# Performance work log

Measured on AMD Instinct MI355X. Metric: run time of the kernel, lower is better.

Reference implementation:

```python
import jax, jax.numpy as jnp
import numpy as np

ROUTING_ITERS = 3
EPS = 1e-07


def setup_inputs() -> dict:
    key = jax.random.key(0)
    k1, k2 = jax.random.split(key)
    B, IN_CAPS, OUT_CAPS, POSE = 128, 2048, 32, 4
    votes = jax.random.normal(k1, (B, IN_CAPS, OUT_CAPS, POSE), dtype=jnp.float32)
    activations_in = jax.random.uniform(k2, (B, IN_CAPS), dtype=jnp.float32)
    return {"votes": votes, "activations_in": activations_in}


def _safe_norm(s, axis=-1):
    # NOTE: original safe_norm always keeps dims (reduce_sum keepdims=True, then sqrt)
    return jnp.sqrt(jnp.sum(jnp.square(s), axis=axis, keepdims=True) + EPS)


def _squash(s):
    s_norm = _safe_norm(s, axis=-1)                 # [..., 1]
    scale = jnp.square(s_norm) / (1.0 + jnp.square(s_norm))
    return scale * (s / s_norm)


def reference(votes, activations_in):
    # votes: [B, in_caps, out_caps, pose]
    B, in_caps, out_caps, _ = votes.shape
    b_ij = jnp.zeros((B, in_caps, out_caps), dtype=jnp.float32)
    v_j = None
    for _ in range(ROUTING_ITERS):
        c_ij = jax.nn.softmax(b_ij, axis=2)                       # [B, I, O]
        s_j = jnp.einsum('bio,biop->bop', c_ij, votes)            # [B, O, P]
        v_j = _squash(s_j)                                        # [B, O, P]
        v_stop = jax.lax.stop_gradient(v_j)
        agreement = jnp.einsum('biop,bop->bio', votes, v_stop)    # [B, I, O]
        b_ij = b_ij + agreement
    poses_out = v_j                                               # [B, O, P]
    activations_out = _safe_norm(poses_out, axis=-1)              # [B, O, 1] (keepdims bug preserved)
    return poses_out, activations_out
```

## Files before the change

kernel.cpp:

```cpp
#include <hip/hip_runtime.h>


#define BATCH 128
#define IC 2048
#define OC 32
#define POSE 4
#define REPS 1e-7f
#define CHUNKS 16
#define CHUNK_I (IC / CHUNKS)
#define BLOCK_T 256
#define GROUPS (BLOCK_T / 32)
#define ILP 4
#define STEPS (CHUNK_I / (GROUPS * ILP))

__device__ __forceinline__ float dot4(const float4 a, const float4 b) {
    return a.x*b.x + a.y*b.y + a.z*b.z + a.w*b.w;
}

__device__ __forceinline__ float4 squash4(const float4 s) {
    const float n2 = s.x*s.x + s.y*s.y + s.z*s.z + s.w*s.w + REPS;
    const float f = n2 / (1.f + n2) * rsqrtf(n2);
    return make_float4(f*s.x, f*s.y, f*s.z, f*s.w);
}

template <int T>
__global__ __launch_bounds__(BLOCK_T) void routing_accum(
    const float4* __restrict__ votes,
    const float4* __restrict__ s_all,
    float* __restrict__ s_out)
{
    const int blk   = blockIdx.x;
    const int b     = blk >> 4;
    const int chunk = blk & (CHUNKS - 1);
    const int o     = threadIdx.x & 31;
    const int g     = threadIdx.x >> 5;

    float4 vh0 = make_float4(0.f, 0.f, 0.f, 0.f);
    float4 vh1 = make_float4(0.f, 0.f, 0.f, 0.f);
    if (T >= 1) vh0 = squash4(s_all[0 * BATCH * OC + b * OC + o]);
    if (T >= 2) vh1 = squash4(s_all[1 * BATCH * OC + b * OC + o]);

    float4 s_acc = make_float4(0.f, 0.f, 0.f, 0.f);

    const float4* vb = votes + (size_t)b * IC * OC;
    const int i0 = chunk * CHUNK_I;

    #pragma unroll
    for (int step = 0; step < STEPS; ++step) {
        const int ia = i0 + step * (GROUPS * ILP) + g;
        float4 v0 = vb[(size_t)(ia + 0 * GROUPS) * OC + o];
        float4 v1 = vb[(size_t)(ia + 1 * GROUPS) * OC + o];
        float4 v2 = vb[(size_t)(ia + 2 * GROUPS) * OC + o];
        float4 v3 = vb[(size_t)(ia + 3 * GROUPS) * OC + o];

        if (T == 0) {
            s_acc.x += (v0.x + v1.x) + (v2.x + v3.x);
            s_acc.y += (v0.y + v1.y) + (v2.y + v3.y);
            s_acc.z += (v0.z + v1.z) + (v2.z + v3.z);
            s_acc.w += (v0.w + v1.w) + (v2.w + v3.w);
        } else {
            float l0 = dot4(v0, vh0);
            float l1 = dot4(v1, vh0);
            float l2 = dot4(v2, vh0);
            float l3 = dot4(v3, vh0);
            if (T >= 2) {
                l0 += dot4(v0, vh1); l1 += dot4(v1, vh1);
                l2 += dot4(v2, vh1); l3 += dot4(v3, vh1);
            }
            float e0 = __expf(l0), e1 = __expf(l1), e2 = __expf(l2), e3 = __expf(l3);
            float t0 = e0, t1 = e1, t2 = e2, t3 = e3;
            #pragma unroll
            for (int d = 16; d >= 1; d >>= 1) {
                t0 += __shfl_xor(t0, d);
                t1 += __shfl_xor(t1, d);
                t2 += __shfl_xor(t2, d);
                t3 += __shfl_xor(t3, d);
            }
            const float c0 = e0 * __builtin_amdgcn_rcpf(t0);
            const float c1 = e1 * __builtin_amdgcn_rcpf(t1);
            const float c2 = e2 * __builtin_amdgcn_rcpf(t2);
            const float c3 = e3 * __builtin_amdgcn_rcpf(t3);

            s_acc.x += c0*v0.x + c1*v1.x + c2*v2.x + c3*v3.x;
            s_acc.y += c0*v0.y + c1*v1.y + c2*v2.y + c3*v3.y;
            s_acc.z += c0*v0.z + c1*v1.z + c2*v2.z + c3*v3.z;
            s_acc.w += c0*v0.w + c1*v1.w + c2*v2.w + c3*v3.w;
        }
    }

    __shared__ float4 lds_s[GROUPS * 32];
    lds_s[g * 32 + o] = s_acc;
    __syncthreads();

    if (threadIdx.x < 32) {
        float4 tot = lds_s[o];
        #pragma unroll
        for (int gg = 1; gg < GROUPS; ++gg) {
            const float4 x = lds_s[gg * 32 + o];
            tot.x += x.x; tot.y += x.y; tot.z += x.z; tot.w += x.w;
        }
        if (T == 0) {
            const float inv = 1.f / 32.f;
            tot.x *= inv; tot.y *= inv; tot.z *= inv; tot.w *= inv;
        }
        float* dst = s_out + ((size_t)b * OC + o) * 4;
        atomicAdd(dst + 0, tot.x);
        atomicAdd(dst + 1, tot.y);
        atomicAdd(dst + 2, tot.z);
        atomicAdd(dst + 3, tot.w);
    }
}

__global__ void routing_finalize(
    const float4* __restrict__ s2,
    float* __restrict__ out)
{
    const int idx = blockIdx.x * blockDim.x + threadIdx.x;
    if (idx >= BATCH * OC) return;
    const float4 v = squash4(s2[idx]);
    ((float4*)out)[idx] = v;
    const float a = sqrtf(v.x*v.x + v.y*v.y + v.z*v.z + v.w*v.w + REPS);
    out[BATCH * OC * POSE + idx] = a;
}

extern "C" void kernel_launch(void* const* d_in, const int* in_sizes, int n_in,
                              void* d_out, int out_size, void* d_ws, size_t ws_size,
                              hipStream_t stream) {
    const float4* votes = (const float4*)d_in[0];

    float* s_all = (float*)d_ws;

    hipMemsetAsync(s_all, 0, (size_t)3 * BATCH * OC * 4 * sizeof(float), stream);

    const float4* s_all4 = (const float4*)s_all;
    routing_accum<0><<<BATCH * CHUNKS, BLOCK_T, 0, stream>>>(
        votes, s_all4, s_all + 0 * BATCH * OC * 4);
    routing_accum<1><<<BATCH * CHUNKS, BLOCK_T, 0, stream>>>(
        votes, s_all4, s_all + 1 * BATCH * OC * 4);
    routing_accum<2><<<BATCH * CHUNKS, BLOCK_T, 0, stream>>>(
        votes, s_all4, s_all + 2 * BATCH * OC * 4);
    routing_finalize<<<(BATCH * OC + 255) / 256, 256, 0, stream>>>(
        s_all4 + 2 * BATCH * OC, (float*)d_out);
}
```

Measured before the change: 236.7 us.

## Fuse routing passes into one cooperative kernel with grid-wide syncs

Replaces the memset, three accumulation launches and the finalize launch with a single cooperative kernel of 1024 blocks. The blocks zero the workspace, then run the three routing passes with grid.sync barriers between them and finalize the outputs in place. This removes the per-launch overhead and the separate memset, and drops ILP from 4 to 2 to fit the new block count. The cost is several grid-wide barriers, and the kernel only works if all 1024 blocks can be resident at once.

```diff
diff --git a/kernel.cpp b/kernel.cpp
--- a/kernel.cpp
+++ b/kernel.cpp
@@ -1,4 +1,7 @@
 #include <hip/hip_runtime.h>
+#include <hip/hip_cooperative_groups.h>
+
+namespace cg = cooperative_groups;
 
 
 #define BATCH 128
@@ -6,11 +9,12 @@
 #define OC 32
 #define POSE 4
 #define REPS 1e-7f
-#define CHUNKS 16
+#define NBLK 1024
+#define CHUNKS (NBLK / BATCH)
 #define CHUNK_I (IC / CHUNKS)
 #define BLOCK_T 256
 #define GROUPS (BLOCK_T / 32)
-#define ILP 4
+#define ILP 2
 #define STEPS (CHUNK_I / (GROUPS * ILP))
 
 __device__ __forceinline__ float dot4(const float4 a, const float4 b) {
@@ -23,75 +27,49 @@
     return make_float4(f*s.x, f*s.y, f*s.z, f*s.w);
 }
 
+__device__ __forceinline__ float4 load4(const float* p) {
+    return *(const float4*)p;
+}
+
 template <int T>
-__global__ __launch_bounds__(BLOCK_T) void routing_accum(
-    const float4* __restrict__ votes,
-    const float4* __restrict__ s_all,
-    float* __restrict__ s_out)
+__device__ __forceinline__ float4 accum_pass(
+    const float4* __restrict__ vb, int i0, int g, int o,
+    float4 vh0, float4 vh1)
 {
-    const int blk   = blockIdx.x;
-    const int b     = blk >> 4;
-    const int chunk = blk & (CHUNKS - 1);
-    const int o     = threadIdx.x & 31;
-    const int g     = threadIdx.x >> 5;
-
-    float4 vh0 = make_float4(0.f, 0.f, 0.f, 0.f);
-    float4 vh1 = make_float4(0.f, 0.f, 0.f, 0.f);
-    if (T >= 1) vh0 = squash4(s_all[0 * BATCH * OC + b * OC + o]);
-    if (T >= 2) vh1 = squash4(s_all[1 * BATCH * OC + b * OC + o]);
-
-    float4 s_acc = make_float4(0.f, 0.f, 0.f, 0.f);
-
-    const float4* vb = votes + (size_t)b * IC * OC;
-    const int i0 = chunk * CHUNK_I;
-
-    #pragma unroll
+    float4 s = make_float4(0.f, 0.f, 0.f, 0.f);
+    #pragma unroll 4
     for (int step = 0; step < STEPS; ++step) {
         const int ia = i0 + step * (GROUPS * ILP) + g;
-        float4 v0 = vb[(size_t)(ia + 0 * GROUPS) * OC + o];
-        float4 v1 = vb[(size_t)(ia + 1 * GROUPS) * OC + o];
-        float4 v2 = vb[(size_t)(ia + 2 * GROUPS) * OC + o];
-        float4 v3 = vb[(size_t)(ia + 3 * GROUPS) * OC + o];
-
+        const float4 v0 = vb[(size_t)ia * OC + o];
+        const float4 v1 = vb[(size_t)(ia + GROUPS) * OC + o];
         if (T == 0) {
-            s_acc.x += (v0.x + v1.x) + (v2.x + v3.x);
-            s_acc.y += (v0.y + v1.y) + (v2.y + v3.y);
-            s_acc.z += (v0.z + v1.z) + (v2.z + v3.z);
-            s_acc.w += (v0.w + v1.w) + (v2.w + v3.w);
+            s.x += v0.x + v1.x; s.y += v0.y + v1.y;
+            s.z += v0.z + v1.z; s.w += v0.w + v1.w;
         } else {
             float l0 = dot4(v0, vh0);
             float l1 = dot4(v1, vh0);
-            float l2 = dot4(v2, vh0);
-            float l3 = dot4(v3, vh0);
-            if (T >= 2) {
-                l0 += dot4(v0, vh1); l1 += dot4(v1, vh1);
-                l2 += dot4(v2, vh1); l3 += dot4(v3, vh1);
-            }
-            float e0 = __expf(l0), e1 = __expf(l1), e2 = __expf(l2), e3 = __expf(l3);
-            float t0 = e0, t1 = e1, t2 = e2, t3 = e3;
+            if (T >= 2) { l0 += dot4(v0, vh1); l1 += dot4(v1, vh1); }
+            float e0 = __expf(l0), e1 = __expf(l1);
+            float t0 = e0, t1 = e1;
             #pragma unroll
             for (int d = 16; d >= 1; d >>= 1) {
                 t0 += __shfl_xor(t0, d);
                 t1 += __shfl_xor(t1, d);
-                t2 += __shfl_xor(t2, d);
-                t3 += __shfl_xor(t3, d);
             }
             const float c0 = e0 * __builtin_amdgcn_rcpf(t0);
             const float c1 = e1 * __builtin_amdgcn_rcpf(t1);
-            const float c2 = e2 * __builtin_amdgcn_rcpf(t2);
-            const float c3 = e3 * __builtin_amdgcn_rcpf(t3);
-
-            s_acc.x += c0*v0.x + c1*v1.x + c2*v2.x + c3*v3.x;
-            s_acc.y += c0*v0.y + c1*v1.y + c2*v2.y + c3*v3.y;
-            s_acc.z += c0*v0.z + c1*v1.z + c2*v2.z + c3*v3.z;
-            s_acc.w += c0*v0.w + c1*v1.w + c2*v2.w + c3*v3.w;
+            s.x += c0*v0.x + c1*v1.x; s.y += c0*v0.y + c1*v1.y;
+            s.z += c0*v0.z + c1*v1.z; s.w += c0*v0.w + c1*v1.w;
         }
     }
+    return s;
+}
 
-    __shared__ float4 lds_s[GROUPS * 32];
-    lds_s[g * 32 + o] = s_acc;
+__device__ __forceinline__ void reduce_atomic(
+    float4 p, float4* lds_s, float* dst_base, int g, int o, float scale)
+{
+    lds_s[g * 32 + o] = p;
     __syncthreads();
-
     if (threadIdx.x < 32) {
         float4 tot = lds_s[o];
         #pragma unroll
@@ -99,46 +77,82 @@
             const float4 x = lds_s[gg * 32 + o];
             tot.x += x.x; tot.y += x.y; tot.z += x.z; tot.w += x.w;
         }
-        if (T == 0) {
-            const float inv = 1.f / 32.f;
-            tot.x *= inv; tot.y *= inv; tot.z *= inv; tot.w *= inv;
-        }
-        float* dst = s_out + ((size_t)b * OC + o) * 4;
-        atomicAdd(dst + 0, tot.x);
-        atomicAdd(dst + 1, tot.y);
-        atomicAdd(dst + 2, tot.z);
-        atomicAdd(dst + 3, tot.w);
+        float* dst = dst_base + o * 4;
+        atomicAdd(dst + 0, tot.x * scale);
+        atomicAdd(dst + 1, tot.y * scale);
+        atomicAdd(dst + 2, tot.z * scale);
+        atomicAdd(dst + 3, tot.w * scale);
     }
 }
 
-__global__ void routing_finalize(
-    const float4* __restrict__ s2,
+__global__ __launch_bounds__(BLOCK_T, 8) void routing_fused(
+    const float4* __restrict__ votes,
+    float* __restrict__ s_all,
     float* __restrict__ out)
 {
-    const int idx = blockIdx.x * blockDim.x + threadIdx.x;
-    if (idx >= BATCH * OC) return;
-    const float4 v = squash4(s2[idx]);
-    ((float4*)out)[idx] = v;
-    const float a = sqrtf(v.x*v.x + v.y*v.y + v.z*v.z + v.w*v.w + REPS);
-    out[BATCH * OC * POSE + idx] = a;
+    cg::grid_group grid = cg::this_grid();
+
+    const int blk   = blockIdx.x;
+    const int b     = blk >> 3;
+    const int chunk = blk & (CHUNKS - 1);
+    const int o     = threadIdx.x & 31;
+    const int g     = threadIdx.x >> 5;
+
+    if (threadIdx.x < 48) s_all[blk * 48 + threadIdx.x] = 0.f;
+
+    __shared__ float4 lds_s[GROUPS * 32];
+
+    const float4* vb = votes + (size_t)b * IC * OC;
+    const int i0 = chunk * CHUNK_I;
+
+    float4 vh0 = make_float4(0.f, 0.f, 0.f, 0.f);
+    float4 vh1 = vh0;
+
+    float4 p = accum_pass<0>(vb, i0, g, o, vh0, vh1);
+    lds_s[g * 32 + o] = p;
+    grid.sync();
+    if (threadIdx.x < 32) {
+        float4 tot = lds_s[o];
+        #pragma unroll
+        for (int gg = 1; gg < GROUPS; ++gg) {
+            const float4 x = lds_s[gg * 32 + o];
+            tot.x += x.x; tot.y += x.y; tot.z += x.z; tot.w += x.w;
+        }
+        float* dst = s_all + 0 * BATCH * OC * 4 + (b * OC + o) * 4;
+        const float inv = 1.f / 32.f;
+        atomicAdd(dst + 0, tot.x * inv);
+        atomicAdd(dst + 1, tot.y * inv);
+        atomicAdd(dst + 2, tot.z * inv);
+        atomicAdd(dst + 3, tot.w * inv);
+    }
+    grid.sync();
+
+    vh0 = squash4(load4(s_all + 0 * BATCH * OC * 4 + (b * OC + o) * 4));
+    p = accum_pass<1>(vb, i0, g, o, vh0, vh1);
+    reduce_atomic(p, lds_s, s_all + 1 * BATCH * OC * 4 + b * OC * 4, g, o, 1.f);
+    grid.sync();
+
+    vh1 = squash4(load4(s_all + 1 * BATCH * OC * 4 + (b * OC + o) * 4));
+    p = accum_pass<2>(vb, i0, g, o, vh0, vh1);
+    reduce_atomic(p, lds_s, s_all + 2 * BATCH * OC * 4 + b * OC * 4, g, o, 1.f);
+    grid.sync();
+
+    if (chunk == 0 && threadIdx.x < 32) {
+        const float4 v = squash4(load4(s_all + 2 * BATCH * OC * 4 + (b * OC + o) * 4));
+        ((float4*)out)[b * OC + o] = v;
+        const float a = sqrtf(v.x*v.x + v.y*v.y + v.z*v.z + v.w*v.w + REPS);
+        out[BATCH * OC * POSE + b * OC + o] = a;
+    }
 }
 
 extern "C" void kernel_launch(void* const* d_in, const int* in_sizes, int n_in,
                               void* d_out, int out_size, void* d_ws, size_t ws_size,
                               hipStream_t stream) {
     const float4* votes = (const float4*)d_in[0];
+    float* s_all = (float*)d_ws;
+    float* outp  = (float*)d_out;
 
-    float* s_all = (float*)d_ws;
-
-    hipMemsetAsync(s_all, 0, (size_t)3 * BATCH * OC * 4 * sizeof(float), stream);
-
-    const float4* s_all4 = (const float4*)s_all;
-    routing_accum<0><<<BATCH * CHUNKS, BLOCK_T, 0, stream>>>(
-        votes, s_all4, s_all + 0 * BATCH * OC * 4);
-    routing_accum<1><<<BATCH * CHUNKS, BLOCK_T, 0, stream>>>(
-        votes, s_all4, s_all + 1 * BATCH * OC * 4);
-    routing_accum<2><<<BATCH * CHUNKS, BLOCK_T, 0, stream>>>(
-        votes, s_all4, s_all + 2 * BATCH * OC * 4);
-    routing_finalize<<<(BATCH * OC + 255) / 256, 256, 0, stream>>>(
-        s_all4 + 2 * BATCH * OC, (float*)d_out);
+    void* args[] = { (void*)&votes, (void*)&s_all, (void*)&outp };
+    hipLaunchCooperativeKernel((void*)routing_fused, dim3(NBLK), dim3(BLOCK_T),
+                               args, 0, stream);
 }
```

Measured after the change: 659.7 us. 2.79x slower.
